# Kernel optimization log

Measured on AMD Instinct MI355X. Metric: run time of the kernel, lower is better.

Reference implementation:

```python
import jax, jax.numpy as jnp
import numpy as np

B, T, DIM, H, HD = 1, 4096, 1024, 8, 128
ATTN_SCALE = 0.12


def _rms_norm(x):
    # F.rms_norm with default eps = finfo(dtype).eps, no learned weight
    eps = jnp.asarray(jnp.finfo(x.dtype).eps, x.dtype)
    return x * jax.lax.rsqrt(jnp.mean(x * x, axis=-1, keepdims=True) + eps)


def _rotary(x):
    # x: [B, T, H, D]; half-rotary: last D/2 freqs are zero (identity)
    t, d = x.shape[1], x.shape[-1]
    freqs = (1.0 / 1024.0) ** jnp.linspace(0.0, 1.0, d // 4, dtype=jnp.float32)
    freqs = jnp.concatenate([freqs, jnp.zeros(d // 4, dtype=jnp.float32)])
    theta = jnp.arange(t, dtype=jnp.float32)[:, None] * freqs[None, :]  # [T, D/2]
    cos = jnp.cos(theta)[None, :, None, :]
    sin = jnp.sin(theta)[None, :, None, :]
    x1, x2 = jnp.split(x.astype(jnp.float32), 2, axis=-1)
    y = jnp.concatenate([x1 * cos + x2 * sin, -x1 * sin + x2 * cos], axis=-1)
    return y.astype(x.dtype)


def setup_inputs() -> dict:
    key = jax.random.key(0)
    k1, k2, k3, k4, k5 = jax.random.split(key, 5)
    std = 0.5 * DIM ** -0.5
    bound = (3.0 ** 0.5) * std
    x = jax.random.normal(k1, (B, T, DIM), dtype=jnp.float32)
    ve = jax.random.normal(k2, (B, T, DIM), dtype=jnp.float32)
    qkv_w = jax.random.uniform(k3, (3, H * HD, DIM), dtype=jnp.float32,
                               minval=-bound, maxval=bound)
    lambdas = jnp.array([0.5, 0.5], dtype=jnp.float32)
    # c_proj is zero-initialized in the source; use small random weights so the
    # output (and gradients) are non-trivial for correctness testing
    c_proj_w = jax.random.normal(k4, (DIM, H * HD), dtype=jnp.float32) * 0.02
    docs = jnp.sort(jax.random.randint(k5, (T,), 0, 8, dtype=jnp.int32))
    return {"x": x, "ve": ve, "qkv_w": qkv_w, "lambdas": lambdas,
            "c_proj_w": c_proj_w, "docs": docs}


def reference(x, ve, qkv_w, lambdas, c_proj_w, docs):
    b, t, _ = x.shape
    w = qkv_w.reshape(3 * H * HD, -1)              # [3*hdim, dim]
    qkv = (x @ w.T).reshape(b, t, 3, H, HD)        # chunk(3, dim=-2) == axis 2 here
    q, k, v = qkv[:, :, 0], qkv[:, :, 1], qkv[:, :, 2]
    q, k = _rms_norm(q), _rms_norm(k)
    q, k = _rotary(q), _rotary(k)
    v = lambdas[0] * v + lambdas[1] * ve.reshape(v.shape)
    # doc-causal mask: attend within the same document, causally
    i = jnp.arange(t)
    mask = (i[:, None] >= i[None, :]) & (docs[:, None] == docs[None, :])  # [T, T]
    scores = jnp.einsum('bihd,bjhd->bhij', q, k) * ATTN_SCALE
    scores = jnp.where(mask[None, None], scores, -jnp.inf)
    p = jax.nn.softmax(scores, axis=-1)
    y = jnp.einsum('bhij,bjhd->bihd', p, v).reshape(b, t, H * HD)
    return y @ c_proj_w.T
```

## Files before the change

### kernel.cpp

```cpp
#include <hip/hip_runtime.h>
#include <hip/hip_bf16.h>
#include <cstdint>

typedef __attribute__((ext_vector_type(8))) short sh8;
typedef __attribute__((ext_vector_type(4))) float f4;

#define T_SEQ 4096
#define DIMN  1024
#define NH    8
#define HDIM  128
#define NQKV  3072
#define ATTN_SCALE 0.12f

__device__ __forceinline__ ushort f2bf(float x) {
  __hip_bfloat16 b = __float2bfloat16(x);
  return *reinterpret_cast<ushort*>(&b);
}
__device__ __forceinline__ float bf2f(ushort u) {
  uint v = ((uint)u) << 16;
  float f;
  __builtin_memcpy(&f, &v, 4);
  return f;
}

#define GLDS16(g, l) \
  __builtin_amdgcn_global_load_lds((const __attribute__((address_space(1))) void*)(g), \
                                   (__attribute__((address_space(3))) void*)(l), 16, 0, 0)

template <int N>
__device__ __forceinline__ void wait_vmcnt() {
  if constexpr (N == 0)      asm volatile("s_waitcnt vmcnt(0)" ::: "memory");
  else if constexpr (N == 4) asm volatile("s_waitcnt vmcnt(4)" ::: "memory");
  else if constexpr (N == 6) asm volatile("s_waitcnt vmcnt(6)" ::: "memory");
  else if constexpr (N == 8) asm volatile("s_waitcnt vmcnt(8)" ::: "memory");
  __builtin_amdgcn_sched_barrier(0);
}

__global__ __launch_bounds__(256) void k_prep(const float* __restrict__ x,
                                              const float* __restrict__ qw,
                                              const float* __restrict__ cw,
                                              ushort* __restrict__ xb, ushort* __restrict__ wb,
                                              ushort* __restrict__ cbuf,
                                              const int* __restrict__ docs, int* __restrict__ dstart) {
  const int b = blockIdx.x;
  if (b < 8192) {
    const int i = b * 256 + threadIdx.x;
    const float* src;
    ushort* dst;
    int j;
    if (i < 1048576)       { src = x;  dst = xb;   j = i; }
    else if (i < 1835008)  { src = qw; dst = wb;   j = i - 1048576; }
    else                   { src = cw; dst = cbuf; j = i - 1835008; }
    float4 v = reinterpret_cast<const float4*>(src)[j];
    ushort4 o;
    o.x = f2bf(v.x); o.y = f2bf(v.y); o.z = f2bf(v.z); o.w = f2bf(v.w);
    reinterpret_cast<ushort4*>(dst)[j] = o;
  } else {
    const int i = (b - 8192) * 256 + threadIdx.x;
    if (i < T_SEQ) {
      int d = docs[i];
      int lo = 0, hi = i;
      while (lo < hi) { int mid = (lo + hi) >> 1; if (docs[mid] < d) lo = mid + 1; else hi = mid; }
      dstart[i] = lo;
    }
  }
}

template <int BM, int BN, int WM, int WN, typename OT>
__global__ __launch_bounds__(WM * WN * 64) void k_gemm2(const ushort* __restrict__ A,
                                                        const ushort* __restrict__ B,
                                                        OT* __restrict__ C,
                                                        int N, int K, int gx) {
  constexpr int NW  = WM * WN;
  constexpr int CHA = BM * 4;
  constexpr int CHT = (BM + BN) * 4;
  constexpr int LPW = CHT / (NW * 64);
  constexpr int TILEB = (BM + BN) * 64;
  constexpr int MF = BM / WM / 16;
  constexpr int NF = BN / WN / 16;

  __shared__ __attribute__((aligned(16))) char lds[3 * TILEB];

  const int tid = threadIdx.x;
  const int lane = tid & 63;
  const int w = tid >> 6;
  const int lr = lane & 15, lg = lane >> 4;
  const int wm = w / WN, wn = w % WN;

  const int nwg = gridDim.x;
  const int nb = (blockIdx.x & 7) * (nwg >> 3) + (blockIdx.x >> 3);
  const int m0 = (nb / gx) * BM;
  const int n0 = (nb % gx) * BN;

  const f4 fzero = {0.f, 0.f, 0.f, 0.f};
  f4 acc[MF][NF];
#pragma unroll
  for (int i = 0; i < MF; ++i)
#pragma unroll
    for (int j = 0; j < NF; ++j) acc[i][j] = fzero;

  const int NT = K >> 5;

  auto STAGE = [&](int t, int buf) {
    const int k0 = t << 5;
#pragma unroll
    for (int l = 0; l < LPW; ++l) {
      const int cb = (l * NW + w) * 64;
      const int ch = cb + lane;
      const ushort* src;
      if (ch < CHA) {
        const int row = ch >> 2;
        const int cs = (ch & 3) ^ ((row >> 1) & 3);
        src = A + (size_t)(m0 + row) * K + k0 + cs * 8;
      } else {
        const int c2 = ch - CHA;
        const int row = c2 >> 2;
        const int cs = (c2 & 3) ^ ((row >> 1) & 3);
        src = B + (size_t)(n0 + row) * K + k0 + cs * 8;
      }
      GLDS16(src, lds + buf * TILEB + cb * 16);
    }
  };

  STAGE(0, 0);
  STAGE(1, 1);
  wait_vmcnt<LPW>();
  __builtin_amdgcn_s_barrier();

  const int sw4 = (lr >> 1) & 3;
  int bufc = 0;

  for (int t = 0; t < NT; ++t) {
    const bool more = (t + 2) < NT;
    if (more) STAGE(t + 2, bufc == 0 ? 2 : (bufc == 1 ? 0 : 1));

    const char* bb = lds + bufc * TILEB;
    sh8 af[MF], bf[NF];
#pragma unroll
    for (int mt = 0; mt < MF; ++mt) {
      const int row = wm * (BM / WM) + mt * 16 + lr;
      af[mt] = *reinterpret_cast<const sh8*>(bb + (row * 4 + (lg ^ sw4)) * 16);
    }
#pragma unroll
    for (int nt = 0; nt < NF; ++nt) {
      const int row = wn * (BN / WN) + nt * 16 + lr;
      bf[nt] = *reinterpret_cast<const sh8*>(bb + (CHA + row * 4 + (lg ^ sw4)) * 16);
    }
    __builtin_amdgcn_s_setprio(1);
#pragma unroll
    for (int mt = 0; mt < MF; ++mt)
#pragma unroll
      for (int nt = 0; nt < NF; ++nt)
        acc[mt][nt] = __builtin_amdgcn_mfma_f32_16x16x32_bf16(af[mt], bf[nt], acc[mt][nt], 0, 0, 0);
    __builtin_amdgcn_s_setprio(0);

    if (more) wait_vmcnt<LPW>();
    else      wait_vmcnt<0>();
    __builtin_amdgcn_s_barrier();
    bufc = bufc == 2 ? 0 : bufc + 1;
  }

#pragma unroll
  for (int mt = 0; mt < MF; ++mt)
#pragma unroll
    for (int nt = 0; nt < NF; ++nt) {
      const int gcol = n0 + wn * (BN / WN) + nt * 16 + lr;
#pragma unroll
      for (int r = 0; r < 4; ++r) {
        const int grow = m0 + wm * (BM / WM) + mt * 16 + lg * 4 + r;
        if constexpr (sizeof(OT) == 2)
          C[(size_t)grow * N + gcol] = (OT)f2bf(acc[mt][nt][r]);
        else
          C[(size_t)grow * N + gcol] = (OT)acc[mt][nt][r];
      }
    }
}

__global__ __launch_bounds__(256) void k_fuse(const ushort* __restrict__ qkvb,
                                              const float* __restrict__ ve,
                                              const float* __restrict__ lam,
                                              ushort* __restrict__ qh, ushort* __restrict__ kh,
                                              ushort* __restrict__ vh) {
  const int pair = blockIdx.x * 4 + (threadIdx.x >> 6);
  const int t = pair >> 3, h = pair & 7;
  const int l = threadIdx.x & 63;
  const ushort* base = qkvb + (size_t)t * NQKV + h * HDIM + 2 * l;
  uint qu = *reinterpret_cast<const uint*>(base);
  uint ku = *reinterpret_cast<const uint*>(base + 1024);
  uint vu = *reinterpret_cast<const uint*>(base + 2048);
  float q0 = bf2f((ushort)qu), q1 = bf2f((ushort)(qu >> 16));
  float k0 = bf2f((ushort)ku), k1 = bf2f((ushort)(ku >> 16));
  float v0 = bf2f((ushort)vu), v1 = bf2f((ushort)(vu >> 16));
  float sq = q0 * q0 + q1 * q1, sk = k0 * k0 + k1 * k1;
#pragma unroll
  for (int m = 1; m < 64; m <<= 1) { sq += __shfl_xor(sq, m); sk += __shfl_xor(sk, m); }
  const float eps = 1.1920928955078125e-07f;
  float rq = rsqrtf(sq * (1.f / 128.f) + eps);
  float rk = rsqrtf(sk * (1.f / 128.f) + eps);
  q0 *= rq; q1 *= rq; k0 *= rk; k1 *= rk;
  float c0 = 1.f, s0 = 0.f, c1 = 1.f, s1 = 0.f;
  if ((l & 31) < 16) {
    const int f0 = 2 * (l & 31);
    float fr0 = exp2f(-10.f * (float)f0 * (1.f / 31.f));
    float fr1 = exp2f(-10.f * (float)(f0 + 1) * (1.f / 31.f));
    sincosf((float)t * fr0, &s0, &c0);
    sincosf((float)t * fr1, &s1, &c1);
  }
  float qx0 = __shfl_xor(q0, 32), qx1 = __shfl_xor(q1, 32);
  float kx0 = __shfl_xor(k0, 32), kx1 = __shfl_xor(k1, 32);
  const float sgn = (l < 32) ? 1.f : -1.f;
  float qr0 = q0 * c0 + sgn * qx0 * s0;
  float qr1 = q1 * c1 + sgn * qx1 * s1;
  float kr0 = k0 * c0 + sgn * kx0 * s0;
  float kr1 = k1 * c1 + sgn * kx1 * s1;
  const float l0 = lam[0], l1 = lam[1];
  float2 vev = *reinterpret_cast<const float2*>(ve + (size_t)t * DIMN + h * HDIM + 2 * l);
  float vr0 = l0 * v0 + l1 * vev.x;
  float vr1 = l0 * v1 + l1 * vev.y;
  const size_t o = ((size_t)h * T_SEQ + t) * HDIM + 2 * l;
  *reinterpret_cast<uint*>(qh + o) = (uint)f2bf(qr0) | ((uint)f2bf(qr1) << 16);
  *reinterpret_cast<uint*>(kh + o) = (uint)f2bf(kr0) | ((uint)f2bf(kr1) << 16);
  *reinterpret_cast<uint*>(vh + o) = (uint)f2bf(vr0) | ((uint)f2bf(vr1) << 16);
}

__global__ __launch_bounds__(256) void k_vt(const ushort* __restrict__ vh, ushort* __restrict__ vt) {
  const int tb = blockIdx.x, db = blockIdx.y, h = blockIdx.z;
  __shared__ ushort L[64][68];
  const int tid = threadIdx.x;
  const int t0 = tb * 64, d0 = db * 64;
  const size_t ib = ((size_t)h * T_SEQ + t0) * HDIM + d0;
#pragma unroll
  for (int p = 0; p < 4; ++p) {
    const int row = p * 16 + (tid >> 4);
    const int c4 = (tid & 15) * 4;
    ushort4 v = *reinterpret_cast<const ushort4*>(vh + ib + (size_t)row * HDIM + c4);
    *reinterpret_cast<ushort4*>(&L[row][c4]) = v;
  }
  __syncthreads();
  const size_t ob = ((size_t)h * HDIM + d0) * T_SEQ + t0;
#pragma unroll
  for (int p = 0; p < 4; ++p) {
    const int drow = p * 16 + (tid >> 4);
    const int t4 = (tid & 15) * 4;
    ushort4 v;
    v.x = L[t4 + 0][drow]; v.y = L[t4 + 1][drow];
    v.z = L[t4 + 2][drow]; v.w = L[t4 + 3][drow];
    *reinterpret_cast<ushort4*>(vt + ob + (size_t)drow * T_SEQ + t4) = v;
  }
}

__global__ __launch_bounds__(256) void k_attn(const ushort* __restrict__ qh,
                                              const ushort* __restrict__ kh,
                                              const ushort* __restrict__ vt,
                                              const int* __restrict__ doc_start,
                                              ushort* __restrict__ y) {
  const int h  = blockIdx.x;
  const int qb = blockIdx.y;
  const int q0 = qb * 64;
  const int tid  = threadIdx.x;
  const int wave = tid >> 6;
  const int lane = tid & 63;
  const int lr = lane & 15, lg = lane >> 4;

  __shared__ ushort Ks[2][64 * 128];
  __shared__ ushort Vs[2][128 * 64];
  __shared__ ushort Ps[4][16 * 64];

  const ushort* Kg = kh + (size_t)h * T_SEQ * HDIM;
  const ushort* Vg = vt + (size_t)h * HDIM * T_SEQ;

  const int i_me = q0 + wave * 16 + lr;
  sh8 qf[4];
  {
    const ushort* qp = qh + ((size_t)h * T_SEQ + i_me) * HDIM + lg * 8;
#pragma unroll
    for (int c = 0; c < 4; ++c) qf[c] = *reinterpret_cast<const sh8*>(qp + c * 32);
  }
  const int ds_me = doc_start[i_me];
  const int ds_hi = doc_start[q0 + 63];
  const int kb0   = doc_start[q0] >> 6;

  const f4 fzero = {0.f, 0.f, 0.f, 0.f};
  f4 o_acc[8];
#pragma unroll
  for (int i = 0; i < 8; ++i) o_acc[i] = fzero;
  float m_me = -1e30f, l_me = 0.f;

  auto STAGE = [&](int b, int k0) {
#pragma unroll
    for (int p = 0; p < 4; ++p) {
      const int c = p * 256 + tid;
      const int row = c >> 4, cc = c & 15;
      GLDS16(Kg + (size_t)(k0 + row) * HDIM + (cc ^ (row & 7)) * 8,
             &Ks[b][(p * 256 + wave * 64) * 8]);
    }
#pragma unroll
    for (int p = 0; p < 4; ++p) {
      const int c = p * 256 + tid;
      const int d = c >> 3, cc = c & 7;
      GLDS16(Vg + (size_t)d * T_SEQ + k0 + (cc ^ (d & 7)) * 8,
             &Vs[b][(p * 256 + wave * 64) * 8]);
    }
  };

  int cur = 0;
  STAGE(0, kb0 * 64);

  const int sw = (lr & 7) << 4;

  for (int kb = kb0; kb <= qb; ++kb) {
    const int k0 = kb * 64;
    __syncthreads();
    if (kb < qb) STAGE(cur ^ 1, k0 + 64);

    const char* Kb = (const char*)&Ks[cur][0];
    const char* Vb = (const char*)&Vs[cur][0];
    char* Pw = (char*)&Ps[wave][0];

    f4 sacc[4];
#pragma unroll
    for (int jt = 0; jt < 4; ++jt) sacc[jt] = fzero;
#pragma unroll
    for (int jt = 0; jt < 4; ++jt)
#pragma unroll
      for (int c = 0; c < 4; ++c) {
        sh8 kf = *reinterpret_cast<const sh8*>(Kb + (jt * 16 + lr) * 256 + ((c * 64 + lg * 16) ^ sw));
        sacc[jt] = __builtin_amdgcn_mfma_f32_16x16x32_bf16(kf, qf[c], sacc[jt], 0, 0, 0);
      }

    const bool fullblk = (kb < qb) && (ds_hi <= k0);
    float p[4][4];
#pragma unroll
    for (int jt = 0; jt < 4; ++jt)
#pragma unroll
      for (int r = 0; r < 4; ++r) {
        float s = sacc[jt][r] * ATTN_SCALE;
        const int j = k0 + jt * 16 + lg * 4 + r;
        bool valid = fullblk || ((j <= i_me) && (j >= ds_me));
        p[jt][r] = valid ? s : -1e30f;
      }
    float tm = -1e30f;
#pragma unroll
    for (int jt = 0; jt < 4; ++jt) {
      float a = fmaxf(p[jt][0], p[jt][1]), b = fmaxf(p[jt][2], p[jt][3]);
      tm = fmaxf(tm, fmaxf(a, b));
    }
    tm = fmaxf(tm, __shfl_xor(tm, 16));
    tm = fmaxf(tm, __shfl_xor(tm, 32));
    const float mnew = fmaxf(m_me, tm);
    const float sc = __expf(m_me - mnew);
    m_me = mnew;
    float rs = 0.f;
#pragma unroll
    for (int jt = 0; jt < 4; ++jt)
#pragma unroll
      for (int r = 0; r < 4; ++r) {
        float pv = __expf(p[jt][r] - mnew);
        p[jt][r] = pv;
        rs += pv;
      }
    rs += __shfl_xor(rs, 16);
    rs += __shfl_xor(rs, 32);
    l_me = l_me * sc + rs;

#pragma unroll
    for (int jt = 0; jt < 4; ++jt) {
      uint2 u;
      u.x = (uint)f2bf(p[jt][0]) | ((uint)f2bf(p[jt][1]) << 16);
      u.y = (uint)f2bf(p[jt][2]) | ((uint)f2bf(p[jt][3]) << 16);
      *reinterpret_cast<uint2*>(Pw + lr * 128 + ((jt * 32 + lg * 8) ^ sw)) = u;
    }

    float sco[4];
#pragma unroll
    for (int rr = 0; rr < 4; ++rr) sco[rr] = __shfl(sc, lg * 4 + rr);
#pragma unroll
    for (int dt = 0; dt < 8; ++dt)
#pragma unroll
      for (int rr = 0; rr < 4; ++rr) o_acc[dt][rr] *= sco[rr];

#pragma unroll
    for (int ks = 0; ks < 2; ++ks) {
      sh8 pa = *reinterpret_cast<const sh8*>(Pw + lr * 128 + ((ks * 64 + lg * 16) ^ sw));
#pragma unroll
      for (int dt = 0; dt < 8; ++dt) {
        sh8 vf = *reinterpret_cast<const sh8*>(Vb + (dt * 16 + lr) * 128 + ((ks * 64 + lg * 16) ^ sw));
        o_acc[dt] = __builtin_amdgcn_mfma_f32_16x16x32_bf16(pa, vf, o_acc[dt], 0, 0, 0);
      }
    }

    __builtin_amdgcn_s_barrier();
    cur ^= 1;
  }

  float lo[4];
#pragma unroll
  for (int rr = 0; rr < 4; ++rr) lo[rr] = __shfl(l_me, lg * 4 + rr);
#pragma unroll
  for (int dt = 0; dt < 8; ++dt)
#pragma unroll
    for (int rr = 0; rr < 4; ++rr) {
      const int trow = q0 + wave * 16 + lg * 4 + rr;
      y[(size_t)trow * DIMN + h * HDIM + dt * 16 + lr] = f2bf(o_acc[dt][rr] / lo[rr]);
    }
}

extern "C" void kernel_launch(void* const* d_in, const int* in_sizes, int n_in,
                              void* d_out, int out_size, void* d_ws, size_t ws_size,
                              hipStream_t stream) {
  const float* x    = (const float*)d_in[0];
  const float* ve   = (const float*)d_in[1];
  const float* qkvw = (const float*)d_in[2];
  const float* lam  = (const float*)d_in[3];
  const float* cpw  = (const float*)d_in[4];
  const int*   docs = (const int*)d_in[5];
  float* out = (float*)d_out;
  char* ws = (char*)d_ws;

  ushort* qkvb = (ushort*)(ws);
  ushort* xb   = (ushort*)(ws + (24ull << 20));
  ushort* wb   = (ushort*)(ws + (32ull << 20));
  ushort* cb   = (ushort*)(ws + (38ull << 20));
  ushort* qh   = (ushort*)(ws + (40ull << 20));
  ushort* kh   = (ushort*)(ws + (48ull << 20));
  ushort* vh   = (ushort*)(ws + (56ull << 20));
  ushort* vt   = (ushort*)(ws + (64ull << 20));
  ushort* yb   = (ushort*)(ws + (72ull << 20));
  int*  dstart = (int*)(ws + (80ull << 20));

  k_prep<<<8192 + 16, 256, 0, stream>>>(x, qkvw, cpw, xb, wb, cb, docs, dstart);

  k_gemm2<256, 128, 2, 2, ushort><<<384, 256, 0, stream>>>(xb, wb, qkvb, NQKV, DIMN, NQKV / 128);

  k_fuse<<<T_SEQ * NH / 4, 256, 0, stream>>>(qkvb, ve, lam, qh, kh, vh);
  k_vt<<<dim3(T_SEQ / 64, HDIM / 64, NH), 256, 0, stream>>>(vh, vt);

  k_attn<<<dim3(NH, T_SEQ / 64), 256, 0, stream>>>(qh, kh, vt, dstart, yb);

  k_gemm2<128, 128, 2, 2, float><<<256, 256, 0, stream>>>(yb, cb, out, DIMN, DIMN, DIMN / 128);
}
```

Before: 117.7 us.

## Replace QKV GEMM with 256x256 eight-wave ping-pong pipelined kernel

Adds a new QKV projection GEMM that uses 256x256 output tiles with 8 waves per block and double-buffered LDS. Global-to-LDS loads are interleaved in half-tile pieces between MFMA groups, with barriers and setprio so memory and compute overlap. The grid drops from 384 to 192 blocks with an XCD-aware block remap. The larger tile raises reuse per byte loaded, at the cost of fewer blocks than CUs (192 vs 256), heavy register use, and many barriers.

```diff
diff --git a/kernel.cpp b/kernel.cpp
--- a/kernel.cpp
+++ b/kernel.cpp
@@ -35,6 +35,8 @@
   else if constexpr (N == 8) asm volatile("s_waitcnt vmcnt(8)" ::: "memory");
   __builtin_amdgcn_sched_barrier(0);
 }
+#define LGKM0 do { asm volatile("s_waitcnt lgkmcnt(0)" ::: "memory"); __builtin_amdgcn_sched_barrier(0); } while (0)
+#define BAR   __builtin_amdgcn_s_barrier()
 
 __global__ __launch_bounds__(256) void k_prep(const float* __restrict__ x,
                                               const float* __restrict__ qw,
@@ -66,6 +68,124 @@
   }
 }
 
+#define RD_A(buf, mh) do {                                                         \
+  const char* hb_ = (const char*)&lds[buf][wave_m][0];                             \
+  _Pragma("unroll") for (int mt = 0; mt < 4; ++mt) {                               \
+    const int row_ = (mh) * 64 + mt * 16 + lr;                                     \
+    _Pragma("unroll") for (int kk = 0; kk < 2; ++kk)                               \
+      a_cur[mt][kk] = *reinterpret_cast<const sh8*>(                               \
+          hb_ + row_ * 128 + ((((kk << 2) | lg) ^ (lr & 7)) << 4));                \
+  }                                                                                \
+} while (0)
+
+#define RD_B(buf, nh, dst) do {                                                    \
+  const char* hb_ = (const char*)&lds[buf][2 + (wave_n >> 1)][0];                  \
+  _Pragma("unroll") for (int nt = 0; nt < 2; ++nt) {                               \
+    const int row_ = (wave_n & 1) * 64 + (nh) * 32 + nt * 16 + lr;                 \
+    _Pragma("unroll") for (int kk = 0; kk < 2; ++kk)                               \
+      dst[nt][kk] = *reinterpret_cast<const sh8*>(                                 \
+          hb_ + row_ * 128 + ((((kk << 2) | lg) ^ (lr & 7)) << 4));                \
+  }                                                                                \
+} while (0)
+
+#define MFMA16(mh, nh, bb) do {                                                    \
+  __builtin_amdgcn_s_setprio(1);                                                   \
+  _Pragma("unroll") for (int mt = 0; mt < 4; ++mt)                                 \
+  _Pragma("unroll") for (int nt = 0; nt < 2; ++nt)                                 \
+  _Pragma("unroll") for (int kk = 0; kk < 2; ++kk)                                 \
+    acc[(mh) * 4 + mt][(nh) * 2 + nt] = __builtin_amdgcn_mfma_f32_16x16x32_bf16(   \
+        a_cur[mt][kk], bb[nt][kk], acc[(mh) * 4 + mt][(nh) * 2 + nt], 0, 0, 0);    \
+  __builtin_amdgcn_s_setprio(0);                                                   \
+} while (0)
+
+__global__ __launch_bounds__(512, 2) void k_gemm8(const ushort* __restrict__ A,
+                                                  const ushort* __restrict__ B,
+                                                  ushort* __restrict__ C,
+                                                  int N, int K, int gx) {
+  __shared__ ushort lds[2][4][128 * 64];
+  const int tid = threadIdx.x;
+  const int lane = tid & 63;
+  const int w = tid >> 6;
+  const int lr = lane & 15, lg = lane >> 4;
+  const int wave_m = w >> 2, wave_n = w & 3;
+
+  const int nwg = gridDim.x;
+  const int nb = (blockIdx.x & 7) * (nwg >> 3) + (blockIdx.x >> 3);
+  const int m0 = (nb / gx) * 256;
+  const int n0 = (nb % gx) * 256;
+
+  f4 acc[8][4];
+  const f4 fzero = {0.f, 0.f, 0.f, 0.f};
+#pragma unroll
+  for (int i = 0; i < 8; ++i)
+#pragma unroll
+    for (int j = 0; j < 4; ++j) acc[i][j] = fzero;
+
+  auto stage_half = [&](int buf, int half, const ushort* base, int rowb, int k0) {
+#pragma unroll
+    for (int l = 0; l < 2; ++l) {
+      const int chunk = l * 512 + tid;
+      const int row = chunk >> 3, cj = chunk & 7;
+      GLDS16(base + (size_t)(rowb + row) * K + k0 + ((cj ^ (row & 7)) << 3),
+             &lds[buf][half][(l * 512 + w * 64) * 8]);
+    }
+  };
+
+  sh8 a_cur[4][2], b0[2][2], b1[2][2];
+
+  const int NT = K >> 6;
+  const int NP = NT >> 1;
+
+  stage_half(0, 2, B, n0, 0);       stage_half(0, 3, B, n0 + 128, 0);
+  stage_half(0, 0, A, m0, 0);       stage_half(0, 1, A, m0 + 128, 0);
+  stage_half(1, 2, B, n0, 64);      stage_half(1, 3, B, n0 + 128, 64);
+  stage_half(1, 0, A, m0, 64);
+  wait_vmcnt<6>();
+  BAR;
+
+  for (int p = 0; p < NP; ++p) {
+    const int kO  = (p * 2 + 1) << 6;
+    const int kN0 = (p * 2 + 2) << 6;
+    const int kN1 = (p * 2 + 3) << 6;
+    const bool more = (p + 1) < NP;
+
+    RD_A(0, 0); RD_B(0, 0, b0);
+    stage_half(1, 1, A, m0 + 128, kO);
+    BAR; LGKM0; MFMA16(0, 0, b0); BAR;
+    RD_B(0, 1, b1);
+    BAR; LGKM0; MFMA16(0, 1, b1); BAR;
+    RD_A(0, 1);
+    if (more) { stage_half(0, 2, B, n0, kN0); stage_half(0, 3, B, n0 + 128, kN0); }
+    BAR; LGKM0; MFMA16(1, 0, b0); BAR;
+    if (more) { stage_half(0, 0, A, m0, kN0); wait_vmcnt<6>(); }
+    else      { wait_vmcnt<0>(); }
+    BAR; MFMA16(1, 1, b1); BAR;
+    RD_A(1, 0); RD_B(1, 0, b0);
+    if (more) stage_half(0, 1, A, m0 + 128, kN0);
+    BAR; LGKM0; MFMA16(0, 0, b0); BAR;
+    RD_B(1, 1, b1);
+    BAR; LGKM0; MFMA16(0, 1, b1); BAR;
+    RD_A(1, 1);
+    if (more) { stage_half(1, 2, B, n0, kN1); stage_half(1, 3, B, n0 + 128, kN1); }
+    BAR; LGKM0; MFMA16(1, 0, b0); BAR;
+    if (more) stage_half(1, 0, A, m0, kN1);
+    wait_vmcnt<6>();
+    BAR; MFMA16(1, 1, b1); BAR;
+  }
+
+#pragma unroll
+  for (int mf = 0; mf < 8; ++mf)
+#pragma unroll
+    for (int nf = 0; nf < 4; ++nf) {
+      const int gcol = n0 + wave_n * 64 + nf * 16 + lr;
+#pragma unroll
+      for (int r = 0; r < 4; ++r) {
+        const int grow = m0 + wave_m * 128 + mf * 16 + lg * 4 + r;
+        C[(size_t)grow * N + gcol] = f2bf(acc[mf][nf][r]);
+      }
+    }
+}
+
 template <int BM, int BN, int WM, int WN, typename OT>
 __global__ __launch_bounds__(WM * WN * 64) void k_gemm2(const ushort* __restrict__ A,
                                                         const ushort* __restrict__ B,
@@ -430,7 +550,7 @@
 
   k_prep<<<8192 + 16, 256, 0, stream>>>(x, qkvw, cpw, xb, wb, cb, docs, dstart);
 
-  k_gemm2<256, 128, 2, 2, ushort><<<384, 256, 0, stream>>>(xb, wb, qkvb, NQKV, DIMN, NQKV / 128);
+  k_gemm8<<<192, 512, 0, stream>>>(xb, wb, qkvb, NQKV, DIMN, NQKV / 256);
 
   k_fuse<<<T_SEQ * NH / 4, 256, 0, stream>>>(qkvb, ve, lam, qh, kh, vh);
   k_vt<<<dim3(T_SEQ / 64, HDIM / 64, NH), 256, 0, stream>>>(vh, vt);
```

Result: faster. 106.9 us (-9.2%).

## Rewrite QKV GEMM with 128x384 tiles, 8 waves, and 32x32x16 MFMAs

Applied to the files above, without the earlier changes.

Replaces the QKV projection GEMM with a new 512-thread kernel. It uses 128x384 block tiles, a K-step of 64 with double-buffered LDS and split staging, an XOR swizzle, and 32x32x16 bf16 MFMA instructions, launched as 256 blocks. The output-projection GEMM is specialised to 128x128 tiles and also switched to 32x32x16 MFMAs. The aim is more operand reuse per LDS read and fewer MFMA issues. The cost is higher register pressure, and the 32x32 accumulator layout gives a more scattered epilogue store.

```diff
diff --git a/kernel.cpp b/kernel.cpp
--- a/kernel.cpp
+++ b/kernel.cpp
@@ -4,6 +4,7 @@
 
 typedef __attribute__((ext_vector_type(8))) short sh8;
 typedef __attribute__((ext_vector_type(4))) float f4;
+typedef __attribute__((ext_vector_type(16))) float f16v;
 
 #define T_SEQ 4096
 #define DIMN  1024
@@ -35,6 +36,7 @@
   else if constexpr (N == 8) asm volatile("s_waitcnt vmcnt(8)" ::: "memory");
   __builtin_amdgcn_sched_barrier(0);
 }
+#define BAR __builtin_amdgcn_s_barrier()
 
 __global__ __launch_bounds__(256) void k_prep(const float* __restrict__ x,
                                               const float* __restrict__ qw,
@@ -66,38 +68,148 @@
   }
 }
 
-template <int BM, int BN, int WM, int WN, typename OT>
-__global__ __launch_bounds__(WM * WN * 64) void k_gemm2(const ushort* __restrict__ A,
-                                                        const ushort* __restrict__ B,
-                                                        OT* __restrict__ C,
-                                                        int N, int K, int gx) {
-  constexpr int NW  = WM * WN;
-  constexpr int CHA = BM * 4;
-  constexpr int CHT = (BM + BN) * 4;
-  constexpr int LPW = CHT / (NW * 64);
-  constexpr int TILEB = (BM + BN) * 64;
-  constexpr int MF = BM / WM / 16;
-  constexpr int NF = BN / WN / 16;
-
-  __shared__ __attribute__((aligned(16))) char lds[3 * TILEB];
-
+__global__ __launch_bounds__(512, 2) void k_gemm32(const ushort* __restrict__ A,
+                                                   const ushort* __restrict__ B,
+                                                   ushort* __restrict__ C,
+                                                   int N, int K) {
+  __shared__ ushort lds[2][512 * 64];
   const int tid = threadIdx.x;
   const int lane = tid & 63;
   const int w = tid >> 6;
-  const int lr = lane & 15, lg = lane >> 4;
-  const int wm = w / WN, wn = w % WN;
+  const int l5 = lane >> 5;
+  const int lr32 = lane & 31;
+  const int wave_m = w >> 2, wave_n = w & 3;
+
+  const int bid = blockIdx.x;
+  const int s = (bid & 7) * 32 + (bid >> 3);
+  const int m0 = ((s >> 5) * 4 + ((s >> 3) & 3)) * 128;
+  const int n0 = (s & 7) * 384;
+
+  f16v acc[2][3];
+#pragma unroll
+  for (int i = 0; i < 2; ++i)
+#pragma unroll
+    for (int j = 0; j < 3; ++j)
+#pragma unroll
+      for (int r = 0; r < 16; ++r) acc[i][j][r] = 0.f;
+
+  const int NT = K >> 6;
+
+  auto STAGE4 = [&](int buf, int t, int ug) {
+    const int k0 = t << 6;
+#pragma unroll
+    for (int uu = 0; uu < 4; ++uu) {
+      const int u = ug * 4 + uu;
+      const int row = u * 64 + (tid >> 3);
+      const int c = (tid & 7) ^ (row & 7);
+      const ushort* src = (u < 2) ? (A + (size_t)(m0 + row) * K + k0 + c * 8)
+                                  : (B + (size_t)(n0 + row - 128) * K + k0 + c * 8);
+      GLDS16(src, (char*)&lds[buf][0] + u * 8192 + w * 1024);
+    }
+  };
+
+  STAGE4(0, 0, 0); STAGE4(0, 0, 1);
+  wait_vmcnt<0>();
+  BAR;
+
+  int cur = 0;
+  for (int t = 0; t < NT; ++t) {
+    const bool more = (t + 1) < NT;
+    const char* bb = (const char*)&lds[cur][0];
+
+#define RD_FRAGS(ks, a, b)                                                        \
+    _Pragma("unroll") for (int mt = 0; mt < 2; ++mt) {                            \
+      const int row = wave_m * 64 + mt * 32 + lr32;                               \
+      a[mt] = *(const sh8*)(bb + row * 128 + ((((ks) * 2 + l5) ^ (row & 7)) * 16));\
+    }                                                                             \
+    _Pragma("unroll") for (int nt = 0; nt < 3; ++nt) {                            \
+      const int row = 128 + wave_n * 96 + nt * 32 + lr32;                         \
+      b[nt] = *(const sh8*)(bb + row * 128 + ((((ks) * 2 + l5) ^ (row & 7)) * 16));\
+    }
+
+#define MFMA6(a, b)                                                               \
+    __builtin_amdgcn_s_setprio(1);                                                \
+    _Pragma("unroll") for (int mt = 0; mt < 2; ++mt)                              \
+    _Pragma("unroll") for (int nt = 0; nt < 3; ++nt)                              \
+      acc[mt][nt] = __builtin_amdgcn_mfma_f32_32x32x16_bf16(a[mt], b[nt],         \
+                                                            acc[mt][nt], 0, 0, 0);\
+    __builtin_amdgcn_s_setprio(0);
+
+    {
+      sh8 a[2], b[3];
+      RD_FRAGS(0, a, b)
+      if (more) STAGE4(cur ^ 1, t + 1, 0);
+      MFMA6(a, b)
+    }
+    {
+      sh8 a[2], b[3];
+      RD_FRAGS(1, a, b)
+      if (more) STAGE4(cur ^ 1, t + 1, 1);
+      MFMA6(a, b)
+    }
+    BAR;
+    {
+      sh8 a[2], b[3];
+      RD_FRAGS(2, a, b)
+      MFMA6(a, b)
+    }
+    if (more) wait_vmcnt<4>();
+    {
+      sh8 a[2], b[3];
+      RD_FRAGS(3, a, b)
+      MFMA6(a, b)
+    }
+    if (more) wait_vmcnt<0>();
+    BAR;
+    cur ^= 1;
+  }
+#undef RD_FRAGS
+#undef MFMA6
+
+#pragma unroll
+  for (int mt = 0; mt < 2; ++mt)
+#pragma unroll
+    for (int nt = 0; nt < 3; ++nt) {
+      const int gcol = n0 + wave_n * 96 + nt * 32 + lr32;
+#pragma unroll
+      for (int r = 0; r < 16; ++r) {
+        const int grow = m0 + wave_m * 64 + mt * 32 + (r & 3) + 8 * (r >> 2) + 4 * l5;
+        C[(size_t)grow * N + gcol] = f2bf(acc[mt][nt][r]);
+      }
+    }
+}
+
+__global__ __launch_bounds__(256) void k_gemm2(const ushort* __restrict__ A,
+                                               const ushort* __restrict__ B,
+                                               float* __restrict__ C,
+                                               int N, int K, int gx) {
+  constexpr int BM = 128, BN = 128;
+  constexpr int CHA = BM * 4;
+  constexpr int CHT = (BM + BN) * 4;
+  constexpr int LPW = CHT / 256;
+  constexpr int TILEB = (BM + BN) * 64;
+
+  __shared__ __attribute__((aligned(16))) char lds[3 * TILEB];
+
+  const int tid = threadIdx.x;
+  const int lane = tid & 63;
+  const int w = tid >> 6;
+  const int l5 = lane >> 5;
+  const int lr32 = lane & 31;
+  const int wm = w >> 1, wn = w & 1;
 
   const int nwg = gridDim.x;
   const int nb = (blockIdx.x & 7) * (nwg >> 3) + (blockIdx.x >> 3);
   const int m0 = (nb / gx) * BM;
   const int n0 = (nb % gx) * BN;
 
-  const f4 fzero = {0.f, 0.f, 0.f, 0.f};
-  f4 acc[MF][NF];
-#pragma unroll
-  for (int i = 0; i < MF; ++i)
-#pragma unroll
-    for (int j = 0; j < NF; ++j) acc[i][j] = fzero;
+  f16v acc[2][2];
+#pragma unroll
+  for (int i = 0; i < 2; ++i)
+#pragma unroll
+    for (int j = 0; j < 2; ++j)
+#pragma unroll
+      for (int r = 0; r < 16; ++r) acc[i][j][r] = 0.f;
 
   const int NT = K >> 5;
 
@@ -105,7 +217,7 @@
     const int k0 = t << 5;
 #pragma unroll
     for (int l = 0; l < LPW; ++l) {
-      const int cb = (l * NW + w) * 64;
+      const int cb = (l * 4 + w) * 64;
       const int ch = cb + lane;
       const ushort* src;
       if (ch < CHA) {
@@ -125,53 +237,51 @@
   STAGE(0, 0);
   STAGE(1, 1);
   wait_vmcnt<LPW>();
-  __builtin_amdgcn_s_barrier();
-
-  const int sw4 = (lr >> 1) & 3;
+  BAR;
+
   int bufc = 0;
-
   for (int t = 0; t < NT; ++t) {
     const bool more = (t + 2) < NT;
     if (more) STAGE(t + 2, bufc == 0 ? 2 : (bufc == 1 ? 0 : 1));
 
     const char* bb = lds + bufc * TILEB;
-    sh8 af[MF], bf[NF];
-#pragma unroll
-    for (int mt = 0; mt < MF; ++mt) {
-      const int row = wm * (BM / WM) + mt * 16 + lr;
-      af[mt] = *reinterpret_cast<const sh8*>(bb + (row * 4 + (lg ^ sw4)) * 16);
-    }
-#pragma unroll
-    for (int nt = 0; nt < NF; ++nt) {
-      const int row = wn * (BN / WN) + nt * 16 + lr;
-      bf[nt] = *reinterpret_cast<const sh8*>(bb + (CHA + row * 4 + (lg ^ sw4)) * 16);
-    }
-    __builtin_amdgcn_s_setprio(1);
-#pragma unroll
-    for (int mt = 0; mt < MF; ++mt)
-#pragma unroll
-      for (int nt = 0; nt < NF; ++nt)
-        acc[mt][nt] = __builtin_amdgcn_mfma_f32_16x16x32_bf16(af[mt], bf[nt], acc[mt][nt], 0, 0, 0);
-    __builtin_amdgcn_s_setprio(0);
+#pragma unroll
+    for (int ks = 0; ks < 2; ++ks) {
+      sh8 a[2], b[2];
+#pragma unroll
+      for (int mt = 0; mt < 2; ++mt) {
+        const int row = wm * 64 + mt * 32 + lr32;
+        a[mt] = *(const sh8*)(bb + row * 64 + (((ks * 2 + l5) ^ ((row >> 1) & 3)) * 16));
+      }
+#pragma unroll
+      for (int nt = 0; nt < 2; ++nt) {
+        const int row = wn * 64 + nt * 32 + lr32;
+        b[nt] = *(const sh8*)(bb + BM * 64 + row * 64 + (((ks * 2 + l5) ^ ((row >> 1) & 3)) * 16));
+      }
+      __builtin_amdgcn_s_setprio(1);
+#pragma unroll
+      for (int mt = 0; mt < 2; ++mt)
+#pragma unroll
+        for (int nt = 0; nt < 2; ++nt)
+          acc[mt][nt] = __builtin_amdgcn_mfma_f32_32x32x16_bf16(a[mt], b[nt], acc[mt][nt], 0, 0, 0);
+      __builtin_amdgcn_s_setprio(0);
+    }
 
     if (more) wait_vmcnt<LPW>();
     else      wait_vmcnt<0>();
-    __builtin_amdgcn_s_barrier();
+    BAR;
     bufc = bufc == 2 ? 0 : bufc + 1;
   }
 
 #pragma unroll
-  for (int mt = 0; mt < MF; ++mt)
-#pragma unroll
-    for (int nt = 0; nt < NF; ++nt) {
-      const int gcol = n0 + wn * (BN / WN) + nt * 16 + lr;
-#pragma unroll
-      for (int r = 0; r < 4; ++r) {
-        const int grow = m0 + wm * (BM / WM) + mt * 16 + lg * 4 + r;
-        if constexpr (sizeof(OT) == 2)
-          C[(size_t)grow * N + gcol] = (OT)f2bf(acc[mt][nt][r]);
-        else
-          C[(size_t)grow * N + gcol] = (OT)acc[mt][nt][r];
+  for (int mt = 0; mt < 2; ++mt)
+#pragma unroll
+    for (int nt = 0; nt < 2; ++nt) {
+      const int gcol = n0 + wn * 64 + nt * 32 + lr32;
+#pragma unroll
+      for (int r = 0; r < 16; ++r) {
+        const int grow = m0 + wm * 64 + mt * 32 + (r & 3) + 8 * (r >> 2) + 4 * l5;
+        C[(size_t)grow * N + gcol] = acc[mt][nt][r];
       }
     }
 }
@@ -430,12 +540,12 @@
 
   k_prep<<<8192 + 16, 256, 0, stream>>>(x, qkvw, cpw, xb, wb, cb, docs, dstart);
 
-  k_gemm2<256, 128, 2, 2, ushort><<<384, 256, 0, stream>>>(xb, wb, qkvb, NQKV, DIMN, NQKV / 128);
+  k_gemm32<<<256, 512, 0, stream>>>(xb, wb, qkvb, NQKV, DIMN);
 
   k_fuse<<<T_SEQ * NH / 4, 256, 0, stream>>>(qkvb, ve, lam, qh, kh, vh);
   k_vt<<<dim3(T_SEQ / 64, HDIM / 64, NH), 256, 0, stream>>>(vh, vt);
 
   k_attn<<<dim3(NH, T_SEQ / 64), 256, 0, stream>>>(qh, kh, vt, dstart, yb);
 
-  k_gemm2<128, 128, 2, 2, float><<<256, 256, 0, stream>>>(yb, cb, out, DIMN, DIMN, DIMN / 128);
-}
+  k_gemm2<<<256, 256, 0, stream>>>(yb, cb, out, DIMN, DIMN, DIMN / 128);
+}
```

Result: faster. 102.5 us (-12.9%).
